# Kernel tuning notes

Measured on AMD Instinct MI355X. Metric: run time of the kernel, lower is better.

The kernel has to match this reference:

```python
import jax, jax.numpy as jnp
import numpy as np
from jax import lax

B, L, D, F, K = 16, 1024, 384, 1536, 3
MAX_DUR = 10          # clamp on per-token duration (makes output length static)
T_OUT = L * MAX_DUR   # padded expanded length
ALPHA = 1.0
EPS = 1e-5


def conv1d_same(x_ncl, w, b):
    # x_ncl: [B, Cin, L], w: [Cout, Cin, K]
    y = lax.conv_general_dilated(x_ncl, w, window_strides=(1,), padding='SAME',
                                 dimension_numbers=('NCH', 'OIH', 'NCH'))
    return y + b[None, :, None]


def conv_block(x, wA, bA, wB, bB):
    # x: [B, L, D] -> Conv(D->F) ReLU Conv(F->D) ReLU -> [B, L, D]
    h = x.transpose(0, 2, 1)
    h = jax.nn.relu(conv1d_same(h, wA, bA))
    h = jax.nn.relu(conv1d_same(h, wB, bB))
    return h.transpose(0, 2, 1)


def layernorm(x, g, b):
    mu = jnp.mean(x, axis=-1, keepdims=True)
    var = jnp.var(x, axis=-1, keepdims=True)
    return (x - mu) * lax.rsqrt(var + EPS) * g + b


def setup_inputs() -> dict:
    key = jax.random.key(0)
    ks = jax.random.split(key, 8)
    s = 0.02
    return {
        'y': jax.random.normal(ks[0], (B, L, D), jnp.float32),
        'token_lengths': jax.random.randint(ks[1], (B,), 1, L + 1).astype(jnp.int32),
        'w1a': jax.random.normal(ks[2], (F, D, K), jnp.float32) * s,
        'b1a': jnp.zeros((F,), jnp.float32),
        'w1b': jax.random.normal(ks[3], (D, F, K), jnp.float32) * s,
        'b1b': jnp.zeros((D,), jnp.float32),
        'g1': jnp.ones((D,), jnp.float32),
        'be1': jnp.zeros((D,), jnp.float32),
        'w2a': jax.random.normal(ks[4], (F, D, K), jnp.float32) * s,
        'b2a': jnp.zeros((F,), jnp.float32),
        'w2b': jax.random.normal(ks[5], (D, F, K), jnp.float32) * s,
        'b2b': jnp.zeros((D,), jnp.float32),
        'g2': jnp.ones((D,), jnp.float32),
        'be2': jnp.zeros((D,), jnp.float32),
        'wl': jax.random.normal(ks[6], (D, 1), jnp.float32) * s,
        'bl': jnp.zeros((1,), jnp.float32),
    }


def reference(y, token_lengths, w1a, b1a, w1b, b1b, g1, be1,
              w2a, b2a, w2b, b2b, g2, be2, wl, bl):
    # DurationPredictor (eval mode: dropout is identity)
    h = conv_block(y, w1a, b1a, w1b, b1b)
    h = layernorm(h, g1, be1)
    h = conv_block(h, w2a, b2a, w2b, b2b)
    h = layernorm(h, g2, be2)
    preds = h @ wl + bl                      # [B, L, 1]

    # lengths = round(alpha * exp(preds)), masked to valid tokens, clamped
    lns = jnp.round(ALPHA * jnp.exp(preds[..., 0]))
    lns = jnp.clip(lns, 0, MAX_DUR).astype(jnp.int32)        # [B, L]
    mask = jnp.arange(L)[None, :] < token_lengths[:, None]
    lns = jnp.where(mask, lns, 0)

    # ragged repeat_interleave + pad, fully vectorized:
    # output frame t maps to token idx = searchsorted(cumsum(lns), t, 'right')
    csum = jnp.cumsum(lns, axis=1)                            # [B, L]
    totals = csum[:, -1]                                      # [B]
    t = jnp.arange(T_OUT, dtype=jnp.int32)
    idx = jax.vmap(lambda c: jnp.searchsorted(c, t, side='right'))(csum)  # [B, T_OUT]
    idx = jnp.minimum(idx, L - 1)
    gathered = jnp.take_along_axis(y, idx[..., None], axis=1)  # [B, T_OUT, D]
    valid = t[None, :] < totals[:, None]
    enlarged = jnp.where(valid[..., None], gathered, 0.0)
    return enlarged, totals
```

## Files before the change

### kernel.cpp

```cpp
#include <hip/hip_runtime.h>
#include <hip/hip_bf16.h>

#define BB 16
#define LL 1024
#define DD 384
#define FF 1536
#define KK 3
#define T_OUT 10240
#define MAX_DUR 10

#define PADL 1026
#define LO_SCALE 2048.0f
#define LO_INV   4.8828125e-4f

typedef _Float16 f16x8 __attribute__((ext_vector_type(8)));
typedef float    f32x4 __attribute__((ext_vector_type(4)));

__device__ __forceinline__ void gll16(const void* g, void* l) {
    __builtin_amdgcn_global_load_lds(
        (const __attribute__((address_space(1))) void*)g,
        (__attribute__((address_space(3))) void*)l, 16, 0, 0);
}

__device__ __forceinline__ void split_write(float v, _Float16* hi, _Float16* lo, size_t off) {
    _Float16 h = (_Float16)v;
    hi[off] = h;
    lo[off] = (_Float16)((v - (float)h) * LO_SCALE);
}

__device__ __forceinline__ float split_read(const _Float16* hi, const _Float16* lo, size_t off) {
    return (float)hi[off] + (float)lo[off] * LO_INV;
}

__global__ void wfrag_k(const float* __restrict__ w, _Float16* __restrict__ hi,
                        _Float16* __restrict__ lo, int O, int I) {
    int id = blockIdx.x * 256 + threadIdx.x;
    int total = O * 3 * I;
    if (id >= total) return;
    int e = id & 7;
    int lane = (id >> 3) & 63;
    int rest = id >> 9;
    int nKT = (3 * I) >> 5;
    int ktl = rest % nKT;
    int ot = rest / nKT;
    int o = ot * 16 + (lane & 15);
    int koff = ((lane >> 4) << 3) + e;
    int kseg = ktl % 3;
    int i = (ktl / 3) * 32 + koff;
    float v = w[(o * I + i) * 3 + kseg];
    split_write(v, hi, lo, id);
}

__global__ void ysplit_k(const float* __restrict__ y, _Float16* __restrict__ hi,
                         _Float16* __restrict__ lo) {
    int id = blockIdx.x * 256 + threadIdx.x;
    if (id >= BB * PADL * DD) return;
    int d = id % DD;
    int r = id / DD;
    int b = r / PADL;
    int lr = r - b * PADL;
    float v = 0.f;
    if (lr >= 1 && lr <= LL) v = y[((size_t)(b << 10) + (lr - 1)) * DD + d];
    split_write(v, hi, lo, id);
}

__global__ void padzero_k(_Float16* __restrict__ hi, _Float16* __restrict__ lo, int width) {
    int id = blockIdx.x * 256 + threadIdx.x;
    if (id >= BB * 2 * width) return;
    int b = id / (2 * width);
    int rem = id - b * 2 * width;
    int row = (rem / width) ? (PADL - 1) : 0;
    int c = rem % width;
    size_t off = (size_t)(b * PADL + row) * width + c;
    hi[off] = (_Float16)0.f;
    lo[off] = (_Float16)0.f;
}

__global__ __launch_bounds__(256, 2) void gemm_split(
        const _Float16* __restrict__ Ahi, const _Float16* __restrict__ Alo,
        const _Float16* __restrict__ WfH, const _Float16* __restrict__ WfL,
        const float* __restrict__ bias,
        _Float16* __restrict__ Ohi, _Float16* __restrict__ Olo,
        int Cin, int Cout, int Ktot, int nN) {
    __shared__ _Float16 lds_h[16384];
    const int tid = threadIdx.x;
    const int lane = tid & 63;
    const int w = tid >> 6;
    const int lm = lane & 15, lq = lane >> 4;
    const int xcd = blockIdx.x & 7;
    const int t2 = blockIdx.x >> 3;
    const int g  = t2 / (4 * nN);
    const int r  = t2 - g * (4 * nN);
    const int n_t = r >> 2;
    const int mi  = r & 3;
    const int m_t = ((g * 4 + mi) << 3) + xcd;
    const int m0 = m_t << 7;
    const int n0 = n_t << 7;
    const int b = m0 >> 10;
    const int l0 = m0 & 1023;
    const int rowBase = b * PADL + l0;
    const int wm = (w >> 1) * 64, wn = (w & 1) * 64;

    f32x4 accM[4][4], accC[4][4];
    const f32x4 zz = {0.f, 0.f, 0.f, 0.f};
    #pragma unroll
    for (int i = 0; i < 4; ++i)
        #pragma unroll
        for (int jj = 0; jj < 4; ++jj) { accM[i][jj] = zz; accC[i][jj] = zz; }

    const int nKT = Ktot >> 5;

    auto stageA = [&](int kt, int nxt) {
        int kseg = kt % 3;
        int d0 = (kt / 3) << 5;
        #pragma unroll
        for (int it = 0; it < 2; ++it) {
            int s = (w * 2 + it) * 64 + lane;
            int p = s >> 3, sl = s & 7;
            int t = sl ^ (p & 7);
            int m = p * 2 + (t >> 2);
            int k8 = t & 3;
            size_t aoff = (size_t)(rowBase + m + kseg) * Cin + d0 + k8 * 8;
            _Float16* lbase = lds_h + nxt * 8192 + (size_t)(w * 2 + it) * 512;
            gll16(Ahi + aoff, lbase);
            gll16(Alo + aoff, lbase + 4096);
        }
    };

    auto loadB = [&](int kt, f16x8* bH, f16x8* bL) {
        int ktc = kt < nKT ? kt : nKT - 1;
        #pragma unroll
        for (int jj = 0; jj < 4; ++jj) {
            int ntg = (n0 + wn + jj * 16) >> 4;
            size_t boff = (((size_t)ntg * nKT + ktc) * 64 + lane) * 8;
            bH[jj] = *(const f16x8*)(WfH + boff);
            bL[jj] = *(const f16x8*)(WfL + boff);
        }
    };

    auto compute = [&](const _Float16* lb, const f16x8* bH, const f16x8* bL) {
        #pragma unroll
        for (int i = 0; i < 4; ++i) {
            int m = wm + i * 16 + lm;
            int p = m >> 1;
            int sl = (((m & 1) << 2) | lq) ^ (p & 7);
            int off = p * 64 + sl * 8;
            f16x8 aH = *(const f16x8*)(lb + off);
            f16x8 aL = *(const f16x8*)(lb + 4096 + off);
            #pragma unroll
            for (int jj = 0; jj < 4; ++jj) {
                accM[i][jj] = __builtin_amdgcn_mfma_f32_16x16x32_f16(aH, bH[jj], accM[i][jj], 0, 0, 0);
                accC[i][jj] = __builtin_amdgcn_mfma_f32_16x16x32_f16(aH, bL[jj], accC[i][jj], 0, 0, 0);
                accC[i][jj] = __builtin_amdgcn_mfma_f32_16x16x32_f16(aL, bH[jj], accC[i][jj], 0, 0, 0);
            }
        }
    };

    f16x8 b0H[4], b0L[4], b1H[4], b1L[4];
    loadB(0, b0H, b0L);
    stageA(0, 0);
    for (int kt = 0; kt < nKT; kt += 2) {
        __syncthreads();
        loadB(kt + 1, b1H, b1L);
        if (kt + 1 < nKT) stageA(kt + 1, 1);
        compute(lds_h, b0H, b0L);
        __syncthreads();
        loadB(kt + 2, b0H, b0L);
        if (kt + 2 < nKT) stageA(kt + 2, 0);
        if (kt + 1 < nKT) compute(lds_h + 8192, b1H, b1L);
    }
    #pragma unroll
    for (int i = 0; i < 4; ++i)
        #pragma unroll
        for (int jj = 0; jj < 4; ++jj) {
            int n_g = n0 + wn + jj * 16 + lm;
            float bv = bias[n_g];
            #pragma unroll
            for (int rr = 0; rr < 4; ++rr) {
                int l = l0 + wm + i * 16 + lq * 4 + rr;
                float v = accM[i][jj][rr] + accC[i][jj][rr] * LO_INV + bv;
                v = fmaxf(v, 0.f);
                size_t off = (size_t)(b * PADL + 1 + l) * Cout + n_g;
                split_write(v, Ohi, Olo, off);
            }
        }
}

__global__ __launch_bounds__(128) void ln_split_k(
        _Float16* __restrict__ hi, _Float16* __restrict__ lo,
        const float* __restrict__ g, const float* __restrict__ be) {
    const int row = blockIdx.x;
    const int b = row >> 10, l = row & 1023;
    const size_t base = (size_t)(b * PADL + 1 + l) * DD;
    const int tid = threadIdx.x;
    float v0 = split_read(hi, lo, base + tid);
    float v1 = split_read(hi, lo, base + tid + 128);
    float v2 = split_read(hi, lo, base + tid + 256);

    __shared__ float sh[2];
    float s = v0 + v1 + v2;
    #pragma unroll
    for (int o = 32; o > 0; o >>= 1) s += __shfl_down(s, o, 64);
    if ((tid & 63) == 0) sh[tid >> 6] = s;
    __syncthreads();
    float mu = (sh[0] + sh[1]) * (1.f / DD);
    __syncthreads();
    float d0 = v0 - mu, d1 = v1 - mu, d2 = v2 - mu;
    float q = d0 * d0 + d1 * d1 + d2 * d2;
    #pragma unroll
    for (int o = 32; o > 0; o >>= 1) q += __shfl_down(q, o, 64);
    if ((tid & 63) == 0) sh[tid >> 6] = q;
    __syncthreads();
    float var = (sh[0] + sh[1]) * (1.f / DD);
    float rs = rsqrtf(var + 1e-5f);
    split_write(d0 * rs * g[tid] + be[tid], hi, lo, base + tid);
    split_write(d1 * rs * g[tid + 128] + be[tid + 128], hi, lo, base + tid + 128);
    split_write(d2 * rs * g[tid + 256] + be[tid + 256], hi, lo, base + tid + 256);
}

__global__ __launch_bounds__(128) void ln_pred_split_k(
        const _Float16* __restrict__ hi, const _Float16* __restrict__ lo,
        const float* __restrict__ g, const float* __restrict__ be,
        const float* __restrict__ wl, const float* __restrict__ bl,
        const int* __restrict__ token_lengths, int* __restrict__ lns) {
    const int row = blockIdx.x;
    const int b = row >> 10, l = row & 1023;
    const size_t base = (size_t)(b * PADL + 1 + l) * DD;
    const int tid = threadIdx.x;
    float v0 = split_read(hi, lo, base + tid);
    float v1 = split_read(hi, lo, base + tid + 128);
    float v2 = split_read(hi, lo, base + tid + 256);

    __shared__ float sh[2];
    float s = v0 + v1 + v2;
    #pragma unroll
    for (int o = 32; o > 0; o >>= 1) s += __shfl_down(s, o, 64);
    if ((tid & 63) == 0) sh[tid >> 6] = s;
    __syncthreads();
    float mu = (sh[0] + sh[1]) * (1.f / DD);
    __syncthreads();
    float d0 = v0 - mu, d1 = v1 - mu, d2 = v2 - mu;
    float q = d0 * d0 + d1 * d1 + d2 * d2;
    #pragma unroll
    for (int o = 32; o > 0; o >>= 1) q += __shfl_down(q, o, 64);
    if ((tid & 63) == 0) sh[tid >> 6] = q;
    __syncthreads();
    float var = (sh[0] + sh[1]) * (1.f / DD);
    float rs = rsqrtf(var + 1e-5f);
    __syncthreads();
    float p = (d0 * rs * g[tid]       + be[tid])       * wl[tid]
            + (d1 * rs * g[tid + 128] + be[tid + 128]) * wl[tid + 128]
            + (d2 * rs * g[tid + 256] + be[tid + 256]) * wl[tid + 256];
    #pragma unroll
    for (int o = 32; o > 0; o >>= 1) p += __shfl_down(p, o, 64);
    if ((tid & 63) == 0) sh[tid >> 6] = p;
    __syncthreads();
    if (tid == 0) {
        float pred = sh[0] + sh[1] + bl[0];
        float e = expf(pred);
        float r = rintf(e);
        r = fminf(fmaxf(r, 0.f), (float)MAX_DUR);
        int v = (int)r;
        if (l >= token_lengths[b]) v = 0;
        lns[row] = v;
    }
}

__global__ __launch_bounds__(1024) void cumsum_k(
        const int* __restrict__ lns, int* __restrict__ csum,
        float* __restrict__ totals_out) {
    __shared__ int s[1024];
    const int b = blockIdx.x, tid = threadIdx.x;
    s[tid] = lns[(b << 10) + tid];
    __syncthreads();
    #pragma unroll
    for (int o = 1; o < 1024; o <<= 1) {
        int t = (tid >= o) ? s[tid - o] : 0;
        __syncthreads();
        s[tid] += t;
        __syncthreads();
    }
    csum[(b << 10) + tid] = s[tid];
    if (tid == 1023) totals_out[b] = (float)s[1023];
}

__global__ __launch_bounds__(256) void gather_k(
        const float* __restrict__ y, const int* __restrict__ csum,
        float* __restrict__ out) {
    int gid = blockIdx.x * 256 + threadIdx.x;
    int c4 = gid % 96;
    int rest = gid / 96;
    int t = rest % T_OUT;
    int b = rest / T_OUT;
    const int* c = csum + (b << 10);
    int total = c[1023];
    float4 r = make_float4(0.f, 0.f, 0.f, 0.f);
    if (t < total) {
        int lo = 0, hi = 1024;
        while (lo < hi) {
            int mid = (lo + hi) >> 1;
            if (c[mid] <= t) lo = mid + 1; else hi = mid;
        }
        int idx = min(lo, LL - 1);
        r = *(const float4*)(y + ((size_t)((b << 10) + idx)) * DD + (c4 << 2));
    }
    *(float4*)(out + ((size_t)b * T_OUT + t) * DD + (c4 << 2)) = r;
}

extern "C" void kernel_launch(void* const* d_in, const int* in_sizes, int n_in,
                              void* d_out, int out_size, void* d_ws, size_t ws_size,
                              hipStream_t stream) {
    const float* y   = (const float*)d_in[0];
    const int*   tok = (const int*)d_in[1];
    const float* w1a = (const float*)d_in[2];
    const float* b1a = (const float*)d_in[3];
    const float* w1b = (const float*)d_in[4];
    const float* b1b = (const float*)d_in[5];
    const float* g1  = (const float*)d_in[6];
    const float* be1 = (const float*)d_in[7];
    const float* w2a = (const float*)d_in[8];
    const float* b2a = (const float*)d_in[9];
    const float* w2b = (const float*)d_in[10];
    const float* b2b = (const float*)d_in[11];
    const float* g2  = (const float*)d_in[12];
    const float* be2 = (const float*)d_in[13];
    const float* wl  = (const float*)d_in[14];
    const float* bl  = (const float*)d_in[15];

    float* out = (float*)d_out;

    const size_t WN   = (size_t)FF * DD * KK;
    const size_t SN   = (size_t)BB * PADL * DD;
    const size_t H1N  = (size_t)BB * PADL * FF;
    _Float16* p = (_Float16*)d_ws;
    _Float16* Wh1a = p;              _Float16* Wl1a = Wh1a + WN;
    _Float16* Wh1b = Wl1a + WN;      _Float16* Wl1b = Wh1b + WN;
    _Float16* Wh2a = Wl1b + WN;      _Float16* Wl2a = Wh2a + WN;
    _Float16* Wh2b = Wl2a + WN;      _Float16* Wl2b = Wh2b + WN;
    _Float16* Shi  = Wl2b + WN;      _Float16* Slo  = Shi + SN;
    _Float16* H1hi = Slo + SN;       _Float16* H1lo = H1hi + H1N;
    int* lns  = (int*)(H1lo + H1N);
    int* csum = lns + BB * LL;

    const int M = BB * LL;

    {
        int n = FF * DD * KK;
        wfrag_k<<<(n + 255) / 256, 256, 0, stream>>>(w1a, Wh1a, Wl1a, FF, DD);
        wfrag_k<<<(n + 255) / 256, 256, 0, stream>>>(w1b, Wh1b, Wl1b, DD, FF);
        wfrag_k<<<(n + 255) / 256, 256, 0, stream>>>(w2a, Wh2a, Wl2a, FF, DD);
        wfrag_k<<<(n + 255) / 256, 256, 0, stream>>>(w2b, Wh2b, Wl2b, DD, FF);
        int ny = BB * PADL * DD;
        ysplit_k<<<(ny + 255) / 256, 256, 0, stream>>>(y, Shi, Slo);
        int np = BB * 2 * FF;
        padzero_k<<<(np + 255) / 256, 256, 0, stream>>>(H1hi, H1lo, FF);
    }
    gemm_split<<<(FF / 128) * (M / 128), 256, 0, stream>>>(Shi, Slo, Wh1a, Wl1a, b1a, H1hi, H1lo, DD, FF, 3 * DD, FF / 128);
    gemm_split<<<(DD / 128) * (M / 128), 256, 0, stream>>>(H1hi, H1lo, Wh1b, Wl1b, b1b, Shi, Slo, FF, DD, 3 * FF, DD / 128);
    ln_split_k<<<M, 128, 0, stream>>>(Shi, Slo, g1, be1);
    gemm_split<<<(FF / 128) * (M / 128), 256, 0, stream>>>(Shi, Slo, Wh2a, Wl2a, b2a, H1hi, H1lo, DD, FF, 3 * DD, FF / 128);
    gemm_split<<<(DD / 128) * (M / 128), 256, 0, stream>>>(H1hi, H1lo, Wh2b, Wl2b, b2b, Shi, Slo, FF, DD, 3 * FF, DD / 128);
    ln_pred_split_k<<<M, 128, 0, stream>>>(Shi, Slo, g2, be2, wl, bl, tok, lns);
    cumsum_k<<<BB, 1024, 0, stream>>>(lns, csum, out + (size_t)BB * T_OUT * DD);
    {
        long long n = (long long)BB * T_OUT * 96;
        gather_k<<<(int)((n + 255) / 256), 256, 0, stream>>>(y, csum, out);
    }
}
```

Before: 1.030 ms.

## Split-K the F->D convolutions, fuse prep kernels, precompute gather indices

The F->D conv GEMMs are split into two K halves, each writing its own partial output, which doubles the block count for the under-occupied 384-wide GEMM. Bias, ReLU and the partial sum are folded into the following layernorm kernels. The four weight-prep launches and the y-split/pad launches are merged into two kernels, and the GEMM main loop is restructured to stage two K-tiles per phase with a larger LDS buffer. A separate kernel computes one searchsorted index per output frame so the gather no longer repeats the binary search for each of its 96 column chunks. In exchange there is extra partial-buffer traffic and doubled LDS use, which may lower occupancy.

```diff
diff --git a/kernel.cpp b/kernel.cpp
--- a/kernel.cpp
+++ b/kernel.cpp
@@ -32,14 +32,23 @@
     return (float)hi[off] + (float)lo[off] * LO_INV;
 }
 
-__global__ void wfrag_k(const float* __restrict__ w, _Float16* __restrict__ hi,
-                        _Float16* __restrict__ lo, int O, int I) {
+__global__ void prep_w(const float* __restrict__ w1a, const float* __restrict__ w1b,
+                       const float* __restrict__ w2a, const float* __restrict__ w2b,
+                       _Float16* __restrict__ base) {
+    const int total = FF * 3 * DD;
     int id = blockIdx.x * 256 + threadIdx.x;
-    int total = O * 3 * I;
-    if (id >= total) return;
-    int e = id & 7;
-    int lane = (id >> 3) & 63;
-    int rest = id >> 9;
+    int which = id / total;
+    int rid = id - which * total;
+    if (which >= 4) return;
+    const float* w; _Float16 *hi, *lo; int O, I;
+    const size_t WN = (size_t)FF * DD * KK;
+    if (which == 0)      { w = w1a; O = FF; I = DD; hi = base;          lo = base + WN; }
+    else if (which == 1) { w = w1b; O = DD; I = FF; hi = base + 2 * WN; lo = base + 3 * WN; }
+    else if (which == 2) { w = w2a; O = FF; I = DD; hi = base + 4 * WN; lo = base + 5 * WN; }
+    else                 { w = w2b; O = DD; I = FF; hi = base + 6 * WN; lo = base + 7 * WN; }
+    int e = rid & 7;
+    int lane = (rid >> 3) & 63;
+    int rest = rid >> 9;
     int nKT = (3 * I) >> 5;
     int ktl = rest % nKT;
     int ot = rest / nKT;
@@ -48,47 +57,52 @@
     int kseg = ktl % 3;
     int i = (ktl / 3) * 32 + koff;
     float v = w[(o * I + i) * 3 + kseg];
-    split_write(v, hi, lo, id);
-}
-
-__global__ void ysplit_k(const float* __restrict__ y, _Float16* __restrict__ hi,
-                         _Float16* __restrict__ lo) {
+    split_write(v, hi, lo, rid);
+}
+
+__global__ void prep_y(const float* __restrict__ y, _Float16* __restrict__ shi,
+                       _Float16* __restrict__ slo, _Float16* __restrict__ h1hi,
+                       _Float16* __restrict__ h1lo) {
+    const int SNc = BB * PADL * DD;
     int id = blockIdx.x * 256 + threadIdx.x;
-    if (id >= BB * PADL * DD) return;
-    int d = id % DD;
-    int r = id / DD;
-    int b = r / PADL;
-    int lr = r - b * PADL;
-    float v = 0.f;
-    if (lr >= 1 && lr <= LL) v = y[((size_t)(b << 10) + (lr - 1)) * DD + d];
-    split_write(v, hi, lo, id);
-}
-
-__global__ void padzero_k(_Float16* __restrict__ hi, _Float16* __restrict__ lo, int width) {
-    int id = blockIdx.x * 256 + threadIdx.x;
-    if (id >= BB * 2 * width) return;
-    int b = id / (2 * width);
-    int rem = id - b * 2 * width;
-    int row = (rem / width) ? (PADL - 1) : 0;
-    int c = rem % width;
-    size_t off = (size_t)(b * PADL + row) * width + c;
-    hi[off] = (_Float16)0.f;
-    lo[off] = (_Float16)0.f;
+    if (id < SNc) {
+        int d = id % DD;
+        int r = id / DD;
+        int b = r / PADL;
+        int lr = r - b * PADL;
+        float v = 0.f;
+        if (lr >= 1 && lr <= LL) v = y[((size_t)(b << 10) + (lr - 1)) * DD + d];
+        split_write(v, shi, slo, id);
+        return;
+    }
+    int id2 = id - SNc;
+    if (id2 >= BB * 2 * FF) return;
+    int b = id2 / (2 * FF);
+    int rem = id2 - b * 2 * FF;
+    int row = (rem / FF) ? (PADL - 1) : 0;
+    int c = rem % FF;
+    size_t off = (size_t)(b * PADL + row) * FF + c;
+    h1hi[off] = (_Float16)0.f;
+    h1lo[off] = (_Float16)0.f;
 }
 
 __global__ __launch_bounds__(256, 2) void gemm_split(
         const _Float16* __restrict__ Ahi, const _Float16* __restrict__ Alo,
         const _Float16* __restrict__ WfH, const _Float16* __restrict__ WfL,
         const float* __restrict__ bias,
-        _Float16* __restrict__ Ohi, _Float16* __restrict__ Olo,
-        int Cin, int Cout, int Ktot, int nN) {
-    __shared__ _Float16 lds_h[16384];
+        _Float16* __restrict__ O0hi, _Float16* __restrict__ O0lo,
+        _Float16* __restrict__ O1hi, _Float16* __restrict__ O1lo,
+        int Cin, int Cout, int nKTper, int nN, int blocksPerHalf, int doRelu) {
+    __shared__ _Float16 lds_h[32768];
     const int tid = threadIdx.x;
     const int lane = tid & 63;
     const int w = tid >> 6;
     const int lm = lane & 15, lq = lane >> 4;
-    const int xcd = blockIdx.x & 7;
-    const int t2 = blockIdx.x >> 3;
+    const int nKTfull = (3 * Cin) >> 5;
+    const int half = blockIdx.x / blocksPerHalf;
+    const int t2in = blockIdx.x - half * blocksPerHalf;
+    const int xcd = t2in & 7;
+    const int t2 = t2in >> 3;
     const int g  = t2 / (4 * nN);
     const int r  = t2 - g * (4 * nN);
     const int n_t = r >> 2;
@@ -100,6 +114,8 @@
     const int l0 = m0 & 1023;
     const int rowBase = b * PADL + l0;
     const int wm = (w >> 1) * 64, wn = (w & 1) * 64;
+    const int ktBegin = half * nKTper;
+    const int ktEnd = ktBegin + nKTper;
 
     f32x4 accM[4][4], accC[4][4];
     const f32x4 zz = {0.f, 0.f, 0.f, 0.f};
@@ -108,9 +124,7 @@
         #pragma unroll
         for (int jj = 0; jj < 4; ++jj) { accM[i][jj] = zz; accC[i][jj] = zz; }
 
-    const int nKT = Ktot >> 5;
-
-    auto stageA = [&](int kt, int nxt) {
+    auto stageA = [&](int kt, int ph, int sub) {
         int kseg = kt % 3;
         int d0 = (kt / 3) << 5;
         #pragma unroll
@@ -121,24 +135,22 @@
             int m = p * 2 + (t >> 2);
             int k8 = t & 3;
             size_t aoff = (size_t)(rowBase + m + kseg) * Cin + d0 + k8 * 8;
-            _Float16* lbase = lds_h + nxt * 8192 + (size_t)(w * 2 + it) * 512;
+            _Float16* lbase = lds_h + ph * 16384 + sub * 8192 + (w * 2 + it) * 512;
             gll16(Ahi + aoff, lbase);
             gll16(Alo + aoff, lbase + 4096);
         }
     };
-
     auto loadB = [&](int kt, f16x8* bH, f16x8* bL) {
-        int ktc = kt < nKT ? kt : nKT - 1;
         #pragma unroll
         for (int jj = 0; jj < 4; ++jj) {
             int ntg = (n0 + wn + jj * 16) >> 4;
-            size_t boff = (((size_t)ntg * nKT + ktc) * 64 + lane) * 8;
+            size_t boff = (((size_t)ntg * nKTfull + kt) * 64 + lane) * 8;
             bH[jj] = *(const f16x8*)(WfH + boff);
             bL[jj] = *(const f16x8*)(WfL + boff);
         }
     };
-
-    auto compute = [&](const _Float16* lb, const f16x8* bH, const f16x8* bL) {
+    auto compute = [&](int ph, int sub, const f16x8* bH, const f16x8* bL) {
+        const _Float16* lb = lds_h + ph * 16384 + sub * 8192;
         #pragma unroll
         for (int i = 0; i < 4; ++i) {
             int m = wm + i * 16 + lm;
@@ -156,46 +168,52 @@
         }
     };
 
-    f16x8 b0H[4], b0L[4], b1H[4], b1L[4];
-    loadB(0, b0H, b0L);
-    stageA(0, 0);
-    for (int kt = 0; kt < nKT; kt += 2) {
+    f16x8 bH[4], bL[4];
+    stageA(ktBegin, 0, 0);
+    stageA(ktBegin + 1, 0, 1);
+    loadB(ktBegin, bH, bL);
+    int ph = 0;
+    for (int kt = ktBegin; kt < ktEnd; kt += 2) {
         __syncthreads();
-        loadB(kt + 1, b1H, b1L);
-        if (kt + 1 < nKT) stageA(kt + 1, 1);
-        compute(lds_h, b0H, b0L);
-        __syncthreads();
-        loadB(kt + 2, b0H, b0L);
-        if (kt + 2 < nKT) stageA(kt + 2, 0);
-        if (kt + 1 < nKT) compute(lds_h + 8192, b1H, b1L);
-    }
+        if (kt + 2 < ktEnd) { stageA(kt + 2, ph ^ 1, 0); stageA(kt + 3, ph ^ 1, 1); }
+        compute(ph, 0, bH, bL);
+        loadB(kt + 1, bH, bL);
+        compute(ph, 1, bH, bL);
+        if (kt + 2 < ktEnd) loadB(kt + 2, bH, bL);
+        ph ^= 1;
+    }
+    _Float16* oh = half ? O1hi : O0hi;
+    _Float16* ol = half ? O1lo : O0lo;
     #pragma unroll
     for (int i = 0; i < 4; ++i)
         #pragma unroll
         for (int jj = 0; jj < 4; ++jj) {
             int n_g = n0 + wn + jj * 16 + lm;
-            float bv = bias[n_g];
+            float bv = doRelu ? bias[n_g] : 0.f;
             #pragma unroll
             for (int rr = 0; rr < 4; ++rr) {
                 int l = l0 + wm + i * 16 + lq * 4 + rr;
                 float v = accM[i][jj][rr] + accC[i][jj][rr] * LO_INV + bv;
-                v = fmaxf(v, 0.f);
+                if (doRelu) v = fmaxf(v, 0.f);
                 size_t off = (size_t)(b * PADL + 1 + l) * Cout + n_g;
-                split_write(v, Ohi, Olo, off);
+                split_write(v, oh, ol, off);
             }
         }
 }
 
-__global__ __launch_bounds__(128) void ln_split_k(
-        _Float16* __restrict__ hi, _Float16* __restrict__ lo,
-        const float* __restrict__ g, const float* __restrict__ be) {
+__global__ __launch_bounds__(128) void reduce_ln_k(
+        _Float16* __restrict__ P0hi, _Float16* __restrict__ P0lo,
+        const _Float16* __restrict__ P1hi, const _Float16* __restrict__ P1lo,
+        const float* __restrict__ bias, const float* __restrict__ g,
+        const float* __restrict__ be) {
     const int row = blockIdx.x;
     const int b = row >> 10, l = row & 1023;
     const size_t base = (size_t)(b * PADL + 1 + l) * DD;
     const int tid = threadIdx.x;
-    float v0 = split_read(hi, lo, base + tid);
-    float v1 = split_read(hi, lo, base + tid + 128);
-    float v2 = split_read(hi, lo, base + tid + 256);
+    float v0 = split_read(P0hi, P0lo, base + tid)       + split_read(P1hi, P1lo, base + tid)       + bias[tid];
+    float v1 = split_read(P0hi, P0lo, base + tid + 128) + split_read(P1hi, P1lo, base + tid + 128) + bias[tid + 128];
+    float v2 = split_read(P0hi, P0lo, base + tid + 256) + split_read(P1hi, P1lo, base + tid + 256) + bias[tid + 256];
+    v0 = fmaxf(v0, 0.f); v1 = fmaxf(v1, 0.f); v2 = fmaxf(v2, 0.f);
 
     __shared__ float sh[2];
     float s = v0 + v1 + v2;
@@ -213,23 +231,26 @@
     __syncthreads();
     float var = (sh[0] + sh[1]) * (1.f / DD);
     float rs = rsqrtf(var + 1e-5f);
-    split_write(d0 * rs * g[tid] + be[tid], hi, lo, base + tid);
-    split_write(d1 * rs * g[tid + 128] + be[tid + 128], hi, lo, base + tid + 128);
-    split_write(d2 * rs * g[tid + 256] + be[tid + 256], hi, lo, base + tid + 256);
-}
-
-__global__ __launch_bounds__(128) void ln_pred_split_k(
-        const _Float16* __restrict__ hi, const _Float16* __restrict__ lo,
-        const float* __restrict__ g, const float* __restrict__ be,
-        const float* __restrict__ wl, const float* __restrict__ bl,
-        const int* __restrict__ token_lengths, int* __restrict__ lns) {
+    split_write(d0 * rs * g[tid] + be[tid], P0hi, P0lo, base + tid);
+    split_write(d1 * rs * g[tid + 128] + be[tid + 128], P0hi, P0lo, base + tid + 128);
+    split_write(d2 * rs * g[tid + 256] + be[tid + 256], P0hi, P0lo, base + tid + 256);
+}
+
+__global__ __launch_bounds__(128) void reduce_ln_pred_k(
+        const _Float16* __restrict__ P0hi, const _Float16* __restrict__ P0lo,
+        const _Float16* __restrict__ P1hi, const _Float16* __restrict__ P1lo,
+        const float* __restrict__ bias, const float* __restrict__ g,
+        const float* __restrict__ be, const float* __restrict__ wl,
+        const float* __restrict__ bl, const int* __restrict__ token_lengths,
+        int* __restrict__ lns) {
     const int row = blockIdx.x;
     const int b = row >> 10, l = row & 1023;
     const size_t base = (size_t)(b * PADL + 1 + l) * DD;
     const int tid = threadIdx.x;
-    float v0 = split_read(hi, lo, base + tid);
-    float v1 = split_read(hi, lo, base + tid + 128);
-    float v2 = split_read(hi, lo, base + tid + 256);
+    float v0 = split_read(P0hi, P0lo, base + tid)       + split_read(P1hi, P1lo, base + tid)       + bias[tid];
+    float v1 = split_read(P0hi, P0lo, base + tid + 128) + split_read(P1hi, P1lo, base + tid + 128) + bias[tid + 128];
+    float v2 = split_read(P0hi, P0lo, base + tid + 256) + split_read(P1hi, P1lo, base + tid + 256) + bias[tid + 256];
+    v0 = fmaxf(v0, 0.f); v1 = fmaxf(v1, 0.f); v2 = fmaxf(v2, 0.f);
 
     __shared__ float sh[2];
     float s = v0 + v1 + v2;
@@ -284,27 +305,37 @@
     if (tid == 1023) totals_out[b] = (float)s[1023];
 }
 
+__global__ __launch_bounds__(256) void idx_k(
+        const int* __restrict__ csum, int* __restrict__ idxArr) {
+    int id = blockIdx.x * 256 + threadIdx.x;
+    if (id >= BB * T_OUT) return;
+    int b = id / T_OUT, t = id - b * T_OUT;
+    const int* c = csum + (b << 10);
+    int total = c[1023];
+    int r = -1;
+    if (t < total) {
+        int lo = 0, hi = 1024;
+        while (lo < hi) {
+            int mid = (lo + hi) >> 1;
+            if (c[mid] <= t) lo = mid + 1; else hi = mid;
+        }
+        r = min(lo, LL - 1);
+    }
+    idxArr[id] = r;
+}
+
 __global__ __launch_bounds__(256) void gather_k(
-        const float* __restrict__ y, const int* __restrict__ csum,
+        const float* __restrict__ y, const int* __restrict__ idxArr,
         float* __restrict__ out) {
     int gid = blockIdx.x * 256 + threadIdx.x;
     int c4 = gid % 96;
     int rest = gid / 96;
     int t = rest % T_OUT;
     int b = rest / T_OUT;
-    const int* c = csum + (b << 10);
-    int total = c[1023];
-    float4 r = make_float4(0.f, 0.f, 0.f, 0.f);
-    if (t < total) {
-        int lo = 0, hi = 1024;
-        while (lo < hi) {
-            int mid = (lo + hi) >> 1;
-            if (c[mid] <= t) lo = mid + 1; else hi = mid;
-        }
-        int idx = min(lo, LL - 1);
-        r = *(const float4*)(y + ((size_t)((b << 10) + idx)) * DD + (c4 << 2));
-    }
-    *(float4*)(out + ((size_t)b * T_OUT + t) * DD + (c4 << 2)) = r;
+    int r = idxArr[b * T_OUT + t];
+    float4 v = make_float4(0.f, 0.f, 0.f, 0.f);
+    if (r >= 0) v = *(const float4*)(y + ((size_t)((b << 10) + r)) * DD + (c4 << 2));
+    *(float4*)(out + ((size_t)b * T_OUT + t) * DD + (c4 << 2)) = v;
 }
 
 extern "C" void kernel_launch(void* const* d_in, const int* in_sizes, int n_in,
@@ -332,38 +363,43 @@
     const size_t WN   = (size_t)FF * DD * KK;
     const size_t SN   = (size_t)BB * PADL * DD;
     const size_t H1N  = (size_t)BB * PADL * FF;
-    _Float16* p = (_Float16*)d_ws;
-    _Float16* Wh1a = p;              _Float16* Wl1a = Wh1a + WN;
+    _Float16* wsh = (_Float16*)d_ws;
+    _Float16* Wh1a = wsh;            _Float16* Wl1a = Wh1a + WN;
     _Float16* Wh1b = Wl1a + WN;      _Float16* Wl1b = Wh1b + WN;
     _Float16* Wh2a = Wl1b + WN;      _Float16* Wl2a = Wh2a + WN;
     _Float16* Wh2b = Wl2a + WN;      _Float16* Wl2b = Wh2b + WN;
     _Float16* Shi  = Wl2b + WN;      _Float16* Slo  = Shi + SN;
     _Float16* H1hi = Slo + SN;       _Float16* H1lo = H1hi + H1N;
-    int* lns  = (int*)(H1lo + H1N);
-    int* csum = lns + BB * LL;
+    _Float16* P1hi = H1lo + H1N;     _Float16* P1lo = P1hi + SN;
+    int* lns    = (int*)(P1lo + SN);
+    int* csum   = lns + BB * LL;
+    int* idxArr = csum + BB * LL;
 
     const int M = BB * LL;
 
-    {
-        int n = FF * DD * KK;
-        wfrag_k<<<(n + 255) / 256, 256, 0, stream>>>(w1a, Wh1a, Wl1a, FF, DD);
-        wfrag_k<<<(n + 255) / 256, 256, 0, stream>>>(w1b, Wh1b, Wl1b, DD, FF);
-        wfrag_k<<<(n + 255) / 256, 256, 0, stream>>>(w2a, Wh2a, Wl2a, FF, DD);
-        wfrag_k<<<(n + 255) / 256, 256, 0, stream>>>(w2b, Wh2b, Wl2b, DD, FF);
-        int ny = BB * PADL * DD;
-        ysplit_k<<<(ny + 255) / 256, 256, 0, stream>>>(y, Shi, Slo);
-        int np = BB * 2 * FF;
-        padzero_k<<<(np + 255) / 256, 256, 0, stream>>>(H1hi, H1lo, FF);
-    }
-    gemm_split<<<(FF / 128) * (M / 128), 256, 0, stream>>>(Shi, Slo, Wh1a, Wl1a, b1a, H1hi, H1lo, DD, FF, 3 * DD, FF / 128);
-    gemm_split<<<(DD / 128) * (M / 128), 256, 0, stream>>>(H1hi, H1lo, Wh1b, Wl1b, b1b, Shi, Slo, FF, DD, 3 * FF, DD / 128);
-    ln_split_k<<<M, 128, 0, stream>>>(Shi, Slo, g1, be1);
-    gemm_split<<<(FF / 128) * (M / 128), 256, 0, stream>>>(Shi, Slo, Wh2a, Wl2a, b2a, H1hi, H1lo, DD, FF, 3 * DD, FF / 128);
-    gemm_split<<<(DD / 128) * (M / 128), 256, 0, stream>>>(H1hi, H1lo, Wh2b, Wl2b, b2b, Shi, Slo, FF, DD, 3 * FF, DD / 128);
-    ln_pred_split_k<<<M, 128, 0, stream>>>(Shi, Slo, g2, be2, wl, bl, tok, lns);
+    prep_w<<<(4 * FF * 3 * DD) / 256, 256, 0, stream>>>(w1a, w1b, w2a, w2b, wsh);
+    prep_y<<<(int)((SN + BB * 2 * FF + 255) / 256), 256, 0, stream>>>(y, Shi, Slo, H1hi, H1lo);
+
+    gemm_split<<<(M / 128) * (FF / 128), 256, 0, stream>>>(
+        Shi, Slo, Wh1a, Wl1a, b1a, H1hi, H1lo, H1hi, H1lo,
+        DD, FF, (3 * DD) >> 5, FF / 128, (M / 128) * (FF / 128), 1);
+    gemm_split<<<2 * (M / 128) * (DD / 128), 256, 0, stream>>>(
+        H1hi, H1lo, Wh1b, Wl1b, b1b, Shi, Slo, P1hi, P1lo,
+        FF, DD, ((3 * FF) >> 5) / 2, DD / 128, (M / 128) * (DD / 128), 0);
+    reduce_ln_k<<<M, 128, 0, stream>>>(Shi, Slo, P1hi, P1lo, b1b, g1, be1);
+
+    gemm_split<<<(M / 128) * (FF / 128), 256, 0, stream>>>(
+        Shi, Slo, Wh2a, Wl2a, b2a, H1hi, H1lo, H1hi, H1lo,
+        DD, FF, (3 * DD) >> 5, FF / 128, (M / 128) * (FF / 128), 1);
+    gemm_split<<<2 * (M / 128) * (DD / 128), 256, 0, stream>>>(
+        H1hi, H1lo, Wh2b, Wl2b, b2b, Shi, Slo, P1hi, P1lo,
+        FF, DD, ((3 * FF) >> 5) / 2, DD / 128, (M / 128) * (DD / 128), 0);
+    reduce_ln_pred_k<<<M, 128, 0, stream>>>(Shi, Slo, P1hi, P1lo, b2b, g2, be2, wl, bl, tok, lns);
+
     cumsum_k<<<BB, 1024, 0, stream>>>(lns, csum, out + (size_t)BB * T_OUT * DD);
+    idx_k<<<(BB * T_OUT + 255) / 256, 256, 0, stream>>>(csum, idxArr);
     {
         long long n = (long long)BB * T_OUT * 96;
-        gather_k<<<(int)((n + 255) / 256), 256, 0, stream>>>(y, csum, out);
-    }
-}
+        gather_k<<<(int)((n + 255) / 256), 256, 0, stream>>>(y, idxArr, out);
+    }
+}
```

Result: no change. 1.049 ms (+1.8%).
